# Performance work log

Measured on AMD Instinct MI355X. Metric: run time of the kernel, lower is better.

The kernel has to match this reference:

```python
import jax, jax.numpy as jnp
import numpy as np

B, S, IN, OUT, L, R = 2, 8192, 2048, 2048, 4, 32


def setup_inputs() -> dict:
    key = jax.random.key(0)
    ks = jax.random.split(key, 6)
    return {
        "x": jax.random.normal(ks[0], (B, S, IN), dtype=jnp.float32),
        "weight": jax.random.normal(ks[1], (OUT, IN), dtype=jnp.float32) * 0.02,
        "bias": jax.random.normal(ks[2], (OUT,), dtype=jnp.float32) * 0.02,
        "downs": jax.random.normal(ks[3], (L, R, IN), dtype=jnp.float32) * 0.02,
        "ups": jax.random.normal(ks[4], (L, OUT, R), dtype=jnp.float32) * 0.02,
        "scales": jax.random.uniform(ks[5], (L,), dtype=jnp.float32),
    }


def reference(x, weight, bias, downs, ups, scales):
    # Base linear: y = x @ W.T + b
    y = jnp.einsum("bsi,oi->bso", x, weight) + bias
    # Low-rank LoRA deltas, grouped across adapters:
    # tmp[b,s,l,r] = x @ down_l.T ; delta = sum_l scale_l * tmp_l @ up_l.T
    tmp = jnp.einsum("bsi,lri->bslr", x, downs)  # [B,S,L,R]
    tmp = tmp * scales[None, None, :, None]       # fold per-adapter scale
    delta = jnp.einsum("bslr,lor->bso", tmp, ups)  # [B,S,OUT]
    return y + delta
```

## Files before the change

### kernel.cpp

```cpp
#include <hip/hip_runtime.h>

#define M_DIM 16384
#define N_DIM 2048
#define K_DIM 2048
#define L_AD 4
#define R_AD 32

typedef __bf16 bf16_t;
typedef bf16_t bf16x8 __attribute__((ext_vector_type(8)));
typedef bf16_t bf16x4 __attribute__((ext_vector_type(4)));
typedef float f32x4 __attribute__((ext_vector_type(4)));

#define BM 128
#define BN 128
#define BK 64

__device__ __forceinline__ void async_load16(const void* g, void* l) {
  __builtin_amdgcn_global_load_lds(
      (const __attribute__((address_space(1))) unsigned int*)g,
      (__attribute__((address_space(3))) unsigned int*)l, 16, 0, 0);
}

__global__ __launch_bounds__(256) void convert_x_kernel(
    const float* __restrict__ X, bf16_t* __restrict__ Xb) {
  const size_t base = ((size_t)blockIdx.x * 256 + threadIdx.x) * 8;
  f32x4 lo = *(const f32x4*)(X + base);
  f32x4 hi = *(const f32x4*)(X + base + 4);
  bf16x8 v;
  v[0] = (bf16_t)lo[0]; v[1] = (bf16_t)lo[1];
  v[2] = (bf16_t)lo[2]; v[3] = (bf16_t)lo[3];
  v[4] = (bf16_t)hi[0]; v[5] = (bf16_t)hi[1];
  v[6] = (bf16_t)hi[2]; v[7] = (bf16_t)hi[3];
  *(bf16x8*)(Xb + base) = v;
}

__global__ __launch_bounds__(256) void build_weff_kernel(
    const float* __restrict__ W, const float* __restrict__ downs,
    const float* __restrict__ ups, const float* __restrict__ scales,
    bf16_t* __restrict__ weff) {
  __shared__ float up_s[64 * 129];
  __shared__ float down_s[128 * 64];
  const int t = threadIdx.x;
  const int n0 = blockIdx.y * 64;
  const int k0 = blockIdx.x * 64;

  for (int l = 0; l < L_AD; ++l) {
    const float sc = scales[l];
    const float* up_l = ups + (size_t)l * N_DIM * R_AD;
    #pragma unroll
    for (int j = 0; j < 8; ++j) {
      int flat = j * 256 + t;
      int nl = flat >> 5, r = flat & 31;
      up_s[nl * 129 + l * 32 + r] = sc * up_l[(size_t)(n0 + nl) * R_AD + r];
    }
  }
  #pragma unroll
  for (int j = 0; j < 32; ++j) {
    int flat = j * 256 + t;
    int lr = flat >> 6, kk = flat & 63;
    down_s[lr * 64 + kk] = downs[(size_t)lr * K_DIM + k0 + kk];
  }
  __syncthreads();

  const int tn = t >> 4, tk = t & 15;
  float acc[4][4] = {};
  for (int lr = 0; lr < L_AD * R_AD; ++lr) {
    f32x4 b = *(const f32x4*)&down_s[lr * 64 + tk * 4];
    #pragma unroll
    for (int u = 0; u < 4; ++u) {
      float a = up_s[(tn * 4 + u) * 129 + lr];
      #pragma unroll
      for (int v = 0; v < 4; ++v) acc[u][v] += a * b[v];
    }
  }
  #pragma unroll
  for (int u = 0; u < 4; ++u) {
    int n = n0 + tn * 4 + u;
    f32x4 wv = *(const f32x4*)&W[(size_t)n * K_DIM + k0 + tk * 4];
    bf16x4 o;
    #pragma unroll
    for (int v = 0; v < 4; ++v) o[v] = (bf16_t)(acc[u][v] + wv[v]);
    *(bf16x4*)&weff[(size_t)n * K_DIM + k0 + tk * 4] = o;
  }
}

#define BARRIER() __builtin_amdgcn_s_barrier()
#define SCHEDB() __builtin_amdgcn_sched_barrier(0)
#define VMCNT6() asm volatile("s_waitcnt vmcnt(6)" ::: "memory")

__global__ __launch_bounds__(512, 2) void gemm_bf16_256(
    const bf16_t* __restrict__ Xb, const bf16_t* __restrict__ Wb,
    const float* __restrict__ bias, float* __restrict__ out) {
  __shared__ __align__(16) bf16_t sm[2][2][16384];

  const int orig = blockIdx.x;
  const int swz = (orig & 7) * 64 + (orig >> 3);
  const int m0 = (swz >> 3) * 256;
  const int n0 = (swz & 7) * 256;

  const int t = threadIdx.x;
  const int l = t & 63;
  const int w = t >> 6;
  const int wm = w >> 2, wn = w & 3;
  const int col = l & 15, quad = l >> 4;

  const int d0 = w * 64 + l;
  const int row0 = d0 >> 3;
  const int c0 = (d0 & 7) ^ (row0 & 7);
  const bf16_t* Ab = Xb + (size_t)(m0 + row0) * K_DIM + c0 * 8;
  const bf16_t* Bb = Wb + (size_t)(n0 + row0) * K_DIM + c0 * 8;

  const int arow = wm * 128 + col;
  const int brow = wn * 64 + col;

  float bn[4];
  #pragma unroll
  for (int g = 0; g < 4; ++g) bn[g] = bias[n0 + wn * 64 + g * 16 + col];

  f32x4 acc[8][4] = {};
  bf16x8 aA[4][2], bB[4][2];

#define STG(Gb, B_, OP, H, KT)                                                 \
  do {                                                                         \
    async_load16((Gb) + ((size_t)(H)*128) * K_DIM + (size_t)(KT)*64,           \
                 &sm[B_][OP][(H)*8192 + d0 * 8]);                              \
    async_load16((Gb) + ((size_t)(H)*128 + 64) * K_DIM + (size_t)(KT)*64,      \
                 &sm[B_][OP][(H)*8192 + (d0 + 512) * 8]);                      \
  } while (0)

#define RDA(fi, F0, B_)                                                        \
  do {                                                                         \
    const int R_ = arow + ((F0) + (fi)) * 16;                                  \
    const int rl_ = R_ & 127, h_ = R_ >> 7;                                    \
    _Pragma("unroll") for (int ks_ = 0; ks_ < 2; ++ks_) {                      \
      const int sl_ = (ks_ * 4 + quad) ^ (rl_ & 7);                            \
      aA[fi][ks_] =                                                            \
          *(const bf16x8*)&sm[B_][0][h_ * 8192 + (rl_ * 8 + sl_) * 8];         \
    }                                                                          \
  } while (0)

#define RDB(gi, B_)                                                            \
  do {                                                                         \
    const int R_ = brow + (gi) * 16;                                           \
    const int rl_ = R_ & 127, h_ = R_ >> 7;                                    \
    _Pragma("unroll") for (int ks_ = 0; ks_ < 2; ++ks_) {                      \
      const int sl_ = (ks_ * 4 + quad) ^ (rl_ & 7);                            \
      bB[gi][ks_] =                                                            \
          *(const bf16x8*)&sm[B_][1][h_ * 8192 + (rl_ * 8 + sl_) * 8];         \
    }                                                                          \
  } while (0)

#define MF(FA, G0)                                                             \
  do {                                                                         \
    __builtin_amdgcn_s_setprio(1);                                             \
    _Pragma("unroll") for (int f_ = 0; f_ < 4; ++f_)                           \
        _Pragma("unroll") for (int g_ = 0; g_ < 2; ++g_)                       \
            _Pragma("unroll") for (int ks_ = 0; ks_ < 2; ++ks_)                \
                acc[(FA) + f_][(G0) + g_] =                                    \
                    __builtin_amdgcn_mfma_f32_16x16x32_bf16(                   \
                        aA[f_][ks_], bB[(G0) + g_][ks_],                       \
                        acc[(FA) + f_][(G0) + g_], 0, 0, 0);                   \
    __builtin_amdgcn_s_setprio(0);                                             \
  } while (0)

  STG(Bb, 0, 1, 0, 0); STG(Bb, 0, 1, 1, 0);
  STG(Ab, 0, 0, 0, 0); STG(Ab, 0, 0, 1, 0);
  STG(Bb, 1, 1, 0, 1); STG(Bb, 1, 1, 1, 1);
  STG(Ab, 1, 0, 0, 1);
  VMCNT6();
  BARRIER();

  for (int j = 0; j < 16; ++j) {
    const int k1 = 2 * j + 1;
    const int kt2 = (2 * j + 2 < 32) ? 2 * j + 2 : 31;
    const int kt3 = (2 * j + 3 < 32) ? 2 * j + 3 : 31;

    STG(Ab, 1, 0, 1, k1);
    BARRIER(); SCHEDB();
    RDA(0, 0, 0); RDB(0, 0); RDB(1, 0);
    RDA(1, 0, 0); RDA(2, 0, 0); RDA(3, 0, 0);
    MF(0, 0);
    SCHEDB(); BARRIER();
    STG(Bb, 0, 1, 0, kt2);
    BARRIER(); SCHEDB();
    RDB(2, 0); RDB(3, 0);
    MF(0, 2);
    SCHEDB(); BARRIER();
    STG(Bb, 0, 1, 1, kt2);
    BARRIER(); SCHEDB();
    RDA(0, 4, 0); RDA(1, 4, 0); RDA(2, 4, 0); RDA(3, 4, 0);
    MF(4, 2);
    SCHEDB(); BARRIER();
    STG(Ab, 0, 0, 0, kt2);
    BARRIER(); SCHEDB();
    MF(4, 0);
    VMCNT6();
    BARRIER();
    STG(Ab, 0, 0, 1, kt2);
    BARRIER(); SCHEDB();
    RDA(0, 0, 1); RDB(0, 1); RDB(1, 1);
    RDA(1, 0, 1); RDA(2, 0, 1); RDA(3, 0, 1);
    MF(0, 0);
    SCHEDB(); BARRIER();
    STG(Bb, 1, 1, 0, kt3);
    BARRIER(); SCHEDB();
    RDB(2, 1); RDB(3, 1);
    MF(0, 2);
    SCHEDB(); BARRIER();
    STG(Bb, 1, 1, 1, kt3);
    BARRIER(); SCHEDB();
    RDA(0, 4, 1); RDA(1, 4, 1); RDA(2, 4, 1); RDA(3, 4, 1);
    MF(4, 2);
    SCHEDB(); BARRIER();
    STG(Ab, 1, 0, 0, kt3);
    BARRIER(); SCHEDB();
    MF(4, 0);
    VMCNT6();
    BARRIER();
  }

  #pragma unroll
  for (int f = 0; f < 8; ++f) {
    const int m = m0 + wm * 128 + f * 16 + quad * 4;
    #pragma unroll
    for (int g = 0; g < 4; ++g) {
      const int n = n0 + wn * 64 + g * 16 + col;
      float* op = out + (size_t)m * N_DIM + n;
      #pragma unroll
      for (int r = 0; r < 4; ++r) op[(size_t)r * N_DIM] = acc[f][g][r] + bn[g];
    }
  }
#undef STG
#undef RDA
#undef RDB
#undef MF
}

#define SA 72
__global__ __launch_bounds__(256) void lora_gemm_fallback(
    const float* __restrict__ X, const bf16_t* __restrict__ Wb,
    const float* __restrict__ bias, float* __restrict__ out) {
  __shared__ __align__(16) bf16_t As[BM * SA];
  __shared__ __align__(16) bf16_t Bs[BN * BK];

  const int t = threadIdx.x;
  const int lane = t & 63;
  const int wv = t >> 6;
  const int wm = wv >> 1, wn = wv & 1;
  const int col = lane & 15, quad = lane >> 4;
  const int m0 = blockIdx.y * BM;
  const int n0 = blockIdx.x * BN;
  const int srow = t >> 3;
  const int soct = t & 7;

  f32x4 acc[4][4] = {};
  float bn[4];
  #pragma unroll
  for (int j = 0; j < 4; ++j) bn[j] = bias[n0 + wn * 64 + j * 16 + col];

  for (int kt = 0; kt < K_DIM / BK; ++kt) {
    const int kg = kt * BK;
    #pragma unroll
    for (int j = 0; j < 4; ++j) {
      int n = j * 32 + srow;
      int c = soct ^ (n & 7);
      async_load16(Wb + (size_t)(n0 + n) * K_DIM + kg + c * 8,
                   &Bs[(size_t)(j * 256 + t) * 8]);
    }
    #pragma unroll
    for (int j = 0; j < 4; ++j) {
      int m = j * 32 + srow;
      const f32x4* src = (const f32x4*)(X + (size_t)(m0 + m) * K_DIM + kg + soct * 8);
      f32x4 lo = src[0], hi = src[1];
      bf16x8 v;
      v[0] = (bf16_t)lo[0]; v[1] = (bf16_t)lo[1];
      v[2] = (bf16_t)lo[2]; v[3] = (bf16_t)lo[3];
      v[4] = (bf16_t)hi[0]; v[5] = (bf16_t)hi[1];
      v[6] = (bf16_t)hi[2]; v[7] = (bf16_t)hi[3];
      *(bf16x8*)&As[m * SA + soct * 8] = v;
    }
    __syncthreads();

    #pragma unroll
    for (int ks = 0; ks < 2; ++ks) {
      bf16x8 af[4], bfr[4];
      #pragma unroll
      for (int i = 0; i < 4; ++i)
        af[i] = *(const bf16x8*)&As[(wm * 64 + i * 16 + col) * SA + ks * 32 + quad * 8];
      #pragma unroll
      for (int j = 0; j < 4; ++j) {
        int n = wn * 64 + j * 16 + col;
        int p = (ks * 4 + quad) ^ (n & 7);
        bfr[j] = *(const bf16x8*)&Bs[n * BK + p * 8];
      }
      #pragma unroll
      for (int i = 0; i < 4; ++i) {
        #pragma unroll
        for (int j = 0; j < 4; ++j)
          acc[i][j] = __builtin_amdgcn_mfma_f32_16x16x32_bf16(af[i], bfr[j], acc[i][j], 0, 0, 0);
      }
    }
    __syncthreads();
  }

  #pragma unroll
  for (int i = 0; i < 4; ++i) {
    #pragma unroll
    for (int r = 0; r < 4; ++r) {
      int m = m0 + wm * 64 + i * 16 + quad * 4 + r;
      float* orow = out + (size_t)m * N_DIM + n0 + wn * 64 + col;
      #pragma unroll
      for (int j = 0; j < 4; ++j)
        orow[j * 16] = acc[i][j][r] + bn[j];
    }
  }
}

extern "C" void kernel_launch(void* const* d_in, const int* in_sizes, int n_in,
                              void* d_out, int out_size, void* d_ws, size_t ws_size,
                              hipStream_t stream) {
  const float* x      = (const float*)d_in[0];
  const float* weight = (const float*)d_in[1];
  const float* bias   = (const float*)d_in[2];
  const float* downs  = (const float*)d_in[3];
  const float* ups    = (const float*)d_in[4];
  const float* scales = (const float*)d_in[5];
  float* out = (float*)d_out;

  const size_t weff_bytes = (size_t)N_DIM * K_DIM * 2;
  const size_t xb_bytes   = (size_t)M_DIM * K_DIM * 2;
  bf16_t* weff = (bf16_t*)d_ws;

  dim3 g1(K_DIM / 64, N_DIM / 64);
  build_weff_kernel<<<g1, 256, 0, stream>>>(weight, downs, ups, scales, weff);

  if (ws_size >= weff_bytes + xb_bytes) {
    bf16_t* xb = (bf16_t*)((char*)d_ws + weff_bytes);
    const size_t n_elem = (size_t)M_DIM * K_DIM;
    convert_x_kernel<<<(unsigned)(n_elem / (256 * 8)), 256, 0, stream>>>(x, xb);
    gemm_bf16_256<<<dim3((M_DIM / 256) * (N_DIM / 256)), 512, 0, stream>>>(
        xb, weff, bias, out);
  } else {
    dim3 g2(N_DIM / BN, M_DIM / BM);
    lora_gemm_fallback<<<g2, 256, 0, stream>>>(x, weff, bias, out);
  }
}
```

Measured before the change: 367.2 us.

## Restructure GEMM main loop with split A register buffers and fewer barriers

Splits the A-fragment registers into low and high halves so that all A and B fragments for a K-tile are read from LDS before the stage that overwrites them. This allows the number of block-wide barriers per iteration to be roughly halved. The async global-to-LDS staging order changes, the wait count drops from 6 to 4 outstanding loads, and a full drain is added after the loop. The cost is extra VGPRs for the second A buffer, which could press on occupancy at two blocks per CU. The reordered LDS buffer reuse also needs careful checking for races.

```diff
diff --git a/kernel.cpp b/kernel.cpp
--- a/kernel.cpp
+++ b/kernel.cpp
@@ -86,7 +86,8 @@
 
 #define BARRIER() __builtin_amdgcn_s_barrier()
 #define SCHEDB() __builtin_amdgcn_sched_barrier(0)
-#define VMCNT6() asm volatile("s_waitcnt vmcnt(6)" ::: "memory")
+#define VMCNT4() asm volatile("s_waitcnt vmcnt(4)" ::: "memory")
+#define VMCNT0() asm volatile("s_waitcnt vmcnt(0)" ::: "memory")
 
 __global__ __launch_bounds__(512, 2) void gemm_bf16_256(
     const bf16_t* __restrict__ Xb, const bf16_t* __restrict__ Wb,
@@ -118,7 +119,7 @@
   for (int g = 0; g < 4; ++g) bn[g] = bias[n0 + wn * 64 + g * 16 + col];
 
   f32x4 acc[8][4] = {};
-  bf16x8 aA[4][2], bB[4][2];
+  bf16x8 aLo[4][2], aHi[4][2], bB[4][2];
 
 #define STG(Gb, B_, OP, H, KT)                                                 \
   do {                                                                         \
@@ -128,13 +129,13 @@
                  &sm[B_][OP][(H)*8192 + (d0 + 512) * 8]);                      \
   } while (0)
 
-#define RDA(fi, F0, B_)                                                        \
+#define RDA(dst, fi, F0, B_)                                                   \
   do {                                                                         \
     const int R_ = arow + ((F0) + (fi)) * 16;                                  \
     const int rl_ = R_ & 127, h_ = R_ >> 7;                                    \
     _Pragma("unroll") for (int ks_ = 0; ks_ < 2; ++ks_) {                      \
       const int sl_ = (ks_ * 4 + quad) ^ (rl_ & 7);                            \
-      aA[fi][ks_] =                                                            \
+      dst[fi][ks_] =                                                           \
           *(const bf16x8*)&sm[B_][0][h_ * 8192 + (rl_ * 8 + sl_) * 8];         \
     }                                                                          \
   } while (0)
@@ -150,7 +151,7 @@
     }                                                                          \
   } while (0)
 
-#define MF(FA, G0)                                                             \
+#define MF(AARR, FA, G0)                                                       \
   do {                                                                         \
     __builtin_amdgcn_s_setprio(1);                                             \
     _Pragma("unroll") for (int f_ = 0; f_ < 4; ++f_)                           \
@@ -158,7 +159,7 @@
             _Pragma("unroll") for (int ks_ = 0; ks_ < 2; ++ks_)                \
                 acc[(FA) + f_][(G0) + g_] =                                    \
                     __builtin_amdgcn_mfma_f32_16x16x32_bf16(                   \
-                        aA[f_][ks_], bB[(G0) + g_][ks_],                       \
+                        AARR[f_][ks_], bB[(G0) + g_][ks_],                     \
                         acc[(FA) + f_][(G0) + g_], 0, 0, 0);                   \
     __builtin_amdgcn_s_setprio(0);                                             \
   } while (0)
@@ -166,8 +167,7 @@
   STG(Bb, 0, 1, 0, 0); STG(Bb, 0, 1, 1, 0);
   STG(Ab, 0, 0, 0, 0); STG(Ab, 0, 0, 1, 0);
   STG(Bb, 1, 1, 0, 1); STG(Bb, 1, 1, 1, 1);
-  STG(Ab, 1, 0, 0, 1);
-  VMCNT6();
+  VMCNT4();
   BARRIER();
 
   for (int j = 0; j < 16; ++j) {
@@ -175,53 +175,53 @@
     const int kt2 = (2 * j + 2 < 32) ? 2 * j + 2 : 31;
     const int kt3 = (2 * j + 3 < 32) ? 2 * j + 3 : 31;
 
-    STG(Ab, 1, 0, 1, k1);
-    BARRIER(); SCHEDB();
-    RDA(0, 0, 0); RDB(0, 0); RDB(1, 0);
-    RDA(1, 0, 0); RDA(2, 0, 0); RDA(3, 0, 0);
-    MF(0, 0);
-    SCHEDB(); BARRIER();
-    STG(Bb, 0, 1, 0, kt2);
-    BARRIER(); SCHEDB();
+    STG(Ab, 1, 0, 0, k1); SCHEDB();
+    RDA(aLo, 0, 0, 0); RDB(0, 0); RDB(1, 0);
+    RDA(aLo, 1, 0, 0); RDA(aLo, 2, 0, 0); RDA(aLo, 3, 0, 0);
+    SCHEDB();
     RDB(2, 0); RDB(3, 0);
-    MF(0, 2);
-    SCHEDB(); BARRIER();
-    STG(Bb, 0, 1, 1, kt2);
-    BARRIER(); SCHEDB();
-    RDA(0, 4, 0); RDA(1, 4, 0); RDA(2, 4, 0); RDA(3, 4, 0);
-    MF(4, 2);
-    SCHEDB(); BARRIER();
-    STG(Ab, 0, 0, 0, kt2);
-    BARRIER(); SCHEDB();
-    MF(4, 0);
-    VMCNT6();
-    BARRIER();
-    STG(Ab, 0, 0, 1, kt2);
-    BARRIER(); SCHEDB();
-    RDA(0, 0, 1); RDB(0, 1); RDB(1, 1);
-    RDA(1, 0, 1); RDA(2, 0, 1); RDA(3, 0, 1);
-    MF(0, 0);
-    SCHEDB(); BARRIER();
-    STG(Bb, 1, 1, 0, kt3);
-    BARRIER(); SCHEDB();
+    SCHEDB();
+    MF(aLo, 0, 0);
+    SCHEDB(); BARRIER();
+    STG(Ab, 1, 0, 1, k1); SCHEDB();
+    RDA(aHi, 0, 4, 0); RDA(aHi, 1, 4, 0); RDA(aHi, 2, 4, 0); RDA(aHi, 3, 4, 0);
+    SCHEDB();
+    MF(aLo, 0, 2);
+    SCHEDB(); BARRIER();
+    STG(Bb, 0, 1, 0, kt2); SCHEDB();
+    MF(aHi, 4, 2);
+    SCHEDB(); BARRIER();
+    STG(Bb, 0, 1, 1, kt2); SCHEDB();
+    MF(aHi, 4, 0);
+    SCHEDB(); VMCNT4(); BARRIER();
+    STG(Ab, 0, 0, 0, kt2); SCHEDB();
+    RDA(aLo, 0, 0, 1); RDB(0, 1); RDB(1, 1);
+    RDA(aLo, 1, 0, 1); RDA(aLo, 2, 0, 1); RDA(aLo, 3, 0, 1);
+    SCHEDB();
     RDB(2, 1); RDB(3, 1);
-    MF(0, 2);
-    SCHEDB(); BARRIER();
-    STG(Bb, 1, 1, 1, kt3);
-    BARRIER(); SCHEDB();
-    RDA(0, 4, 1); RDA(1, 4, 1); RDA(2, 4, 1); RDA(3, 4, 1);
-    MF(4, 2);
-    SCHEDB(); BARRIER();
-    STG(Ab, 1, 0, 0, kt3);
-    BARRIER(); SCHEDB();
-    MF(4, 0);
-    VMCNT6();
-    BARRIER();
-  }
+    SCHEDB();
+    MF(aLo, 0, 0);
+    SCHEDB(); BARRIER();
+    STG(Ab, 0, 0, 1, kt2); SCHEDB();
+    RDA(aHi, 0, 4, 1); RDA(aHi, 1, 4, 1); RDA(aHi, 2, 4, 1); RDA(aHi, 3, 4, 1);
+    SCHEDB();
+    MF(aLo, 0, 2);
+    SCHEDB(); BARRIER();
+    STG(Bb, 1, 1, 0, kt3); SCHEDB();
+    MF(aHi, 4, 2);
+    SCHEDB(); BARRIER();
+    STG(Bb, 1, 1, 1, kt3); SCHEDB();
+    MF(aHi, 4, 0);
+    SCHEDB(); VMCNT4(); BARRIER();
+  }
+
+  VMCNT0();
+  BARRIER();
 
   #pragma unroll
   for (int f = 0; f < 8; ++f) {
     const int m = m0 + wm * 128 + f * 16 + quad * 4;
+    const bf16x8* dummy = 0; (void)dummy;
     #pragma unroll
     for (int g = 0; g < 4; ++g) {
       const int n = n0 + wn * 64 + g * 16 + col;
```

Result: no change. 370.5 us (+0.9%).
